# Performance work log

Hardware: AMD Instinct MI355X
Metric: run time of the kernel (lower is better)

The kernel has to match this reference:

```python
import jax, jax.numpy as jnp
import numpy as np
import math

D_MODEL = 512
N_HEADS = 8
D_FF = 2048
EPS = 1e-5

def _layernorm(x, g, b):
    m = jnp.mean(x, axis=-1, keepdims=True)
    v = jnp.var(x, axis=-1, keepdims=True)
    return (x - m) * jax.lax.rsqrt(v + EPS) * g + b

def setup_inputs() -> dict:
    key = jax.random.key(0)
    ks = jax.random.split(key, 8)
    d, dff = D_MODEL, D_FF
    s = lambda fan: 1.0 / math.sqrt(fan)
    return {
        "x": jax.random.normal(ks[0], (4, 2048, d), dtype=jnp.float32),
        "w_qkv": jax.random.normal(ks[1], (d, 3 * d), dtype=jnp.float32) * s(d),
        "b_qkv": jnp.zeros((3 * d,), dtype=jnp.float32),
        "w1": jax.random.normal(ks[2], (d, dff), dtype=jnp.float32) * s(d),
        "b1": jnp.zeros((dff,), dtype=jnp.float32),
        "w2": jax.random.normal(ks[3], (dff, d), dtype=jnp.float32) * s(dff),
        "b2": jnp.zeros((d,), dtype=jnp.float32),
        "g1": jnp.ones((d,), dtype=jnp.float32),
        "be1": jnp.zeros((d,), dtype=jnp.float32),
        "g2": jnp.ones((d,), dtype=jnp.float32),
        "be2": jnp.zeros((d,), dtype=jnp.float32),
    }

def reference(x, w_qkv, b_qkv, w1, b1, w2, b2, g1, be1, g2, be2):
    B, L, d = x.shape
    H = N_HEADS
    hd = d // H
    # Faithful to original: scale = 1/sqrt(hd), scores = qk / scale = qk * sqrt(hd)
    inv_scale = math.sqrt(hd)
    qkv = x @ w_qkv + b_qkv            # [B, L, 3d]
    q, k, v = jnp.split(qkv, 3, axis=-1)
    split_heads = lambda t: t.reshape(B, L, H, hd).transpose(0, 2, 1, 3)  # [B,H,L,hd]
    q, k, v = map(split_heads, (q, k, v))
    scores = jnp.einsum('bhqd,bhkd->bhqk', q, k) * inv_scale
    attn = jax.nn.softmax(scores, axis=-1)
    out = jnp.einsum('bhqk,bhkd->bhqd', attn, v)
    out = out.transpose(0, 2, 1, 3).reshape(B, L, d)
    x = _layernorm(x + out, g1, be1)
    ff = jax.nn.relu(x @ w1 + b1) @ w2 + b2
    return _layernorm(x + ff, g2, be2)
```

## Files before the change

kernel.cpp:

```cpp
#include <hip/hip_runtime.h>

typedef _Float16 f16;
typedef _Float16 f16x4 __attribute__((ext_vector_type(4)));
typedef _Float16 f16x8 __attribute__((ext_vector_type(8)));
typedef float    f32x4 __attribute__((ext_vector_type(4)));
typedef float    f32x16 __attribute__((ext_vector_type(16)));
typedef unsigned int u32x4 __attribute__((ext_vector_type(4)));

#define QK_SCALE 11.5416528f

__device__ __forceinline__ void g2l16(const void* g, void* l) {
  __builtin_amdgcn_global_load_lds(
      (__attribute__((address_space(1))) const unsigned int*)g,
      (__attribute__((address_space(3))) unsigned int*)l, 16, 0, 0);
}

__device__ __forceinline__ f32x4 mfma16(f16x8 a, f16x8 b, f32x4 c) {
  return __builtin_amdgcn_mfma_f32_16x16x32_f16(a, b, c, 0, 0, 0);
}
__device__ __forceinline__ f32x16 mfma32(f16x8 a, f16x8 b, f32x16 c) {
  return __builtin_amdgcn_mfma_f32_32x32x16_f16(a, b, c, 0, 0, 0);
}
__device__ __forceinline__ unsigned pkrtz(float a, float b) {
  auto t = __builtin_amdgcn_cvt_pkrtz(a, b);
  return *(unsigned*)&t;
}
__device__ __forceinline__ void swap32(unsigned& a, unsigned& b) {
  asm volatile("v_permlane32_swap_b32 %0, %1" : "+v"(a), "+v"(b));
}

#define WAIT_BARRIER(N)                                        \
  do {                                                         \
    asm volatile("s_waitcnt vmcnt(" #N ")" ::: "memory");      \
    __builtin_amdgcn_sched_barrier(0);                         \
    __builtin_amdgcn_s_barrier();                              \
    __builtin_amdgcn_sched_barrier(0);                         \
  } while (0)

__device__ __forceinline__ int swz64(int row, int c) { return row * 64 + ((c ^ (row & 7)) << 3); }
__device__ __forceinline__ int swz32(int row, int c) { return row * 32 + ((c ^ ((row >> 1) & 3)) << 3); }

__global__ __launch_bounds__(256) void k_split(const float* __restrict__ in,
                                               f16* __restrict__ hi, f16* __restrict__ lo, int n4) {
  int i = blockIdx.x * 256 + threadIdx.x;
  if (i >= n4) return;
  f32x4 v = ((const f32x4*)in)[i];
  f16x4 h, l;
#pragma unroll
  for (int j = 0; j < 4; ++j) {
    f16 hv = (f16)v[j];
    h[j] = hv;
    l[j] = (f16)(v[j] - (float)hv);
  }
  ((f16x4*)hi)[i] = h;
  ((f16x4*)lo)[i] = l;
}

template <bool WLO>
__global__ __launch_bounds__(256) void k_transpose_split(const float* __restrict__ in, int K, int N,
                                                         f16* __restrict__ oh, f16* __restrict__ ol) {
  __shared__ float t[32][33];
  const int tx = threadIdx.x, ty = threadIdx.y;
  const int n0 = blockIdx.x * 32, k0 = blockIdx.y * 32;
#pragma unroll
  for (int j = 0; j < 4; ++j)
    t[ty + j * 8][tx] = in[(size_t)(k0 + ty + j * 8) * N + n0 + tx];
  __syncthreads();
#pragma unroll
  for (int j = 0; j < 4; ++j) {
    float v = t[tx][ty + j * 8];
    f16 hv = (f16)v;
    size_t o = (size_t)(n0 + ty + j * 8) * K + k0 + tx;
    oh[o] = hv;
    if (WLO) ol[o] = (f16)(v - (float)hv);
  }
}

template <int EPI, bool SPLIT>
__global__ __launch_bounds__(256, SPLIT ? 2 : 3) void k_gemm(
    const f16* __restrict__ Ah, const f16* __restrict__ Al,
    const f16* __restrict__ Bh, const f16* __restrict__ Bl,
    const float* __restrict__ bias,
    f16* __restrict__ outH, f16* __restrict__ outH2,
    f16* __restrict__ oqh, f16* __restrict__ oql,
    f16* __restrict__ okh, f16* __restrict__ ovT,
    int M, int N, int K, int ks) {
  constexpr int NBUF = SPLIT ? 2 : 3;
  constexpr int NB = SPLIT ? 2 : 1;
  __shared__ f16 As[NBUF][NB][128 * 32];
  __shared__ f16 Bs[NBUF][NB][128 * 32];

  const int tid = threadIdx.x;
  const int bm = blockIdx.x, bn = blockIdx.y;
  const int bnc = (EPI == 3) ? (bn & 3) : bn;
  const int half = (EPI == 3) ? (bn >> 2) : 0;
  const int hoff = half * 1024;
  const int w = tid >> 6, lane = tid & 63;
  const int wr = w >> 1, wc = w & 1;
  const int lrow = lane & 15, lgrp = lane >> 4;

  const bool useLo = SPLIT && !(EPI == 0 && bn >= 4);

  f32x4 acc[4][4] = {};

  auto stg = [&](int bf, int kt) {
    const int kk = kt << 5;
#pragma unroll
    for (int c = 0; c < 2; ++c) {
      const int i = tid + (c << 8);
      const int row = i >> 2;
      const int gch = ((i & 3) ^ ((i >> 3) & 3)) << 3;
      const size_t aoff = (size_t)(bm * 128 + row) * ks + hoff + kk + gch;
      const size_t boff = (size_t)(bnc * 128 + row) * ks + hoff + kk + gch;
      g2l16(Ah + aoff, &As[bf][0][i * 8]);
      g2l16(Bh + boff, &Bs[bf][0][i * 8]);
      if (SPLIT)
        if (useLo) {
          g2l16(Al + aoff, &As[bf][1][i * 8]);
          g2l16(Bl + boff, &Bs[bf][1][i * 8]);
        }
    }
  };

  auto compute = [&](int bf) {
    f16x8 a0[4], a1[4], b0[4], b1[4];
#pragma unroll
    for (int mf = 0; mf < 4; ++mf) {
      const int off = swz32(wr * 64 + mf * 16 + lrow, lgrp);
      a0[mf] = *(const f16x8*)&As[bf][0][off];
      if (SPLIT)
        if (useLo) a1[mf] = *(const f16x8*)&As[bf][SPLIT ? 1 : 0][off];
    }
#pragma unroll
    for (int nf = 0; nf < 4; ++nf) {
      const int off = swz32(wc * 64 + nf * 16 + lrow, lgrp);
      b0[nf] = *(const f16x8*)&Bs[bf][0][off];
      if (SPLIT)
        if (useLo) b1[nf] = *(const f16x8*)&Bs[bf][SPLIT ? 1 : 0][off];
    }
#pragma unroll
    for (int mf = 0; mf < 4; ++mf)
#pragma unroll
      for (int nf = 0; nf < 4; ++nf) {
        acc[mf][nf] = mfma16(a0[mf], b0[nf], acc[mf][nf]);
        if (SPLIT)
          if (useLo) {
            acc[mf][nf] = mfma16(a0[mf], b1[nf], acc[mf][nf]);
            acc[mf][nf] = mfma16(a1[mf], b0[nf], acc[mf][nf]);
          }
      }
  };

  const int nkt = K >> 5;
  if constexpr (!SPLIT) {
    stg(0, 0);
    stg(1, 1);
    WAIT_BARRIER(4);
    for (int kt = 0; kt < nkt; ++kt) {
      const int cur = kt % 3;
      const bool more2 = (kt + 2 < nkt);
      if (more2) stg((kt + 2) % 3, kt + 2);
      compute(cur);
      if (kt + 1 < nkt) {
        if (more2) WAIT_BARRIER(4);
        else       WAIT_BARRIER(0);
      }
    }
  } else {
    stg(0, 0);
    WAIT_BARRIER(0);
    for (int kt = 0; kt < nkt; ++kt) {
      const int cur = kt & 1;
      if (kt + 1 < nkt) stg(cur ^ 1, kt + 1);
      compute(cur);
      if (kt + 1 < nkt) WAIT_BARRIER(0);
    }
  }

  const int rowbase = bm * 128 + wr * 64 + lgrp * 4;
  const int colbase = bnc * 128 + wc * 64 + lrow;
#pragma unroll
  for (int mf = 0; mf < 4; ++mf) {
#pragma unroll
    for (int nf = 0; nf < 4; ++nf) {
      const int gc = colbase + nf * 16;
      const float bv = (EPI == 3 && half) ? 0.f : bias[gc];
#pragma unroll
      for (int r = 0; r < 4; ++r) {
        const int gr = rowbase + mf * 16 + r;
        const float val = acc[mf][nf][r] + bv;
        if (EPI == 0) {
          const int bb = gr >> 11, tok = gr & 2047;
          const int kind = gc >> 9, hh = (gc >> 6) & 7, dd = gc & 63;
          const size_t bhp = (size_t)((bb << 3) + hh);
          const size_t qidx = (bhp * 2048 + tok) * 64 + dd;
          if (kind == 0) {
            const float sv = val * QK_SCALE;
            const f16 hv = (f16)sv;
            oqh[qidx] = hv; oql[qidx] = (f16)(sv - (float)hv);
          } else if (kind == 1) {
            okh[qidx] = (f16)val;
          } else {
            ovT[(bhp * 64 + dd) * 2048 + tok] = (f16)val;
          }
        } else if (EPI == 1) {
          outH[(size_t)gr * N + gc] = (f16)fmaxf(val, 0.f);
        } else {
          f16* o = half ? outH2 : outH;
          o[(size_t)gr * N + gc] = (f16)val;
        }
      }
    }
  }
}

__global__ __launch_bounds__(256, 2) void k_attn(
    const f16* __restrict__ Qh, const f16* __restrict__ Ql,
    const f16* __restrict__ Kh, const f16* __restrict__ Vt,
    f16* __restrict__ out) {
  __shared__ f16 sK[4][64 * 64], sV[4][64 * 64];

  const int tid = threadIdx.x;
  const int wg = (blockIdx.x & 7) * 64 + (blockIdx.x >> 3);
  const int bh = wg >> 4, qt = wg & 15;
  const int w = tid >> 6, lane = tid & 63;
  const int lh = lane & 31, hh = lane >> 5;

  const int qrow = qt * 128 + w * 32 + lh;
  const size_t qoff = ((size_t)bh * 2048 + qrow) * 64;
  f16x8 qh8[4], ql8[4];
#pragma unroll
  for (int d = 0; d < 4; ++d) {
    const size_t o = qoff + d * 16 + hh * 8;
    qh8[d] = *(const f16x8*)(Qh + o);
    ql8[d] = *(const f16x8*)(Ql + o);
  }

  auto stage = [&](int b, int kt) {
    const size_t koff = ((size_t)bh * 2048 + (size_t)kt * 64) * 64;
    const size_t voff = (size_t)bh * 64 * 2048 + (size_t)kt * 64;
#pragma unroll
    for (int c = 0; c < 2; ++c) {
      const int i = tid + (c << 8);
      const int row = i >> 3;
      const int gch = ((i & 7) ^ (row & 7)) << 3;
      g2l16(Kh + koff + (size_t)row * 64 + gch, &sK[b][i * 8]);
      g2l16(Vt + voff + (size_t)row * 2048 + gch, &sV[b][i * 8]);
    }
  };

  stage(0, 0);
  stage(1, 1);

  float m_run = -3e38f;
  float l_run = 0.f;
  f32x16 oacc[2] = {};
  const f32x16 kZero = {};
  f32x16 sA[2] = {}, sB[2] = {};

  auto qk = [&](f32x16 (&s)[2], int bi) {
    __builtin_amdgcn_s_setprio(1);
    {
      const f16x8 k0 = *(const f16x8*)&sK[bi][swz64(lh, hh)];
      const f16x8 k1 = *(const f16x8*)&sK[bi][swz64(32 + lh, hh)];
      s[0] = mfma32(k0, qh8[0], kZero);
      s[0] = mfma32(k0, ql8[0], s[0]);
      s[1] = mfma32(k1, qh8[0], kZero);
      s[1] = mfma32(k1, ql8[0], s[1]);
    }
#pragma unroll
    for (int d = 1; d < 4; ++d) {
      const f16x8 k0 = *(const f16x8*)&sK[bi][swz64(lh, d * 2 + hh)];
      const f16x8 k1 = *(const f16x8*)&sK[bi][swz64(32 + lh, d * 2 + hh)];
      s[0] = mfma32(k0, qh8[d], s[0]);
      s[0] = mfma32(k0, ql8[d], s[0]);
      s[1] = mfma32(k1, qh8[d], s[1]);
      s[1] = mfma32(k1, ql8[d], s[1]);
    }
    __builtin_amdgcn_s_setprio(0);
  };

  auto sm_pv = [&](f32x16 (&s)[2], int bi) {
    float mt = s[0][0];
#pragma unroll
    for (int r = 0; r < 16; ++r) { mt = fmaxf(mt, s[0][r]); mt = fmaxf(mt, s[1][r]); }
    mt = fmaxf(mt, __shfl_xor(mt, 32, 64));
    float mcur = m_run;
    if (!__all(mt <= mcur + 8.0f)) {
      const float mnew = fmaxf(mcur, mt);
      const float corr = __builtin_amdgcn_exp2f(mcur - mnew);
      m_run = mnew;
      l_run *= corr;
      oacc[0] = oacc[0] * corr;
      oacc[1] = oacc[1] * corr;
      mcur = mnew;
    }
    float ps = 0.f;
    unsigned pk0[8], pk1[8];
#pragma unroll
    for (int i = 0; i < 8; ++i) {
      const float a0 = __builtin_amdgcn_exp2f(s[0][2 * i] - mcur);
      const float a1 = __builtin_amdgcn_exp2f(s[0][2 * i + 1] - mcur);
      const float b0 = __builtin_amdgcn_exp2f(s[1][2 * i] - mcur);
      const float b1 = __builtin_amdgcn_exp2f(s[1][2 * i + 1] - mcur);
      ps += (a0 + a1) + (b0 + b1);
      pk0[i] = pkrtz(a0, a1);
      pk1[i] = pkrtz(b0, b1);
    }
    ps += __shfl_xor(ps, 32, 64);
    l_run += ps;

    swap32(pk0[0], pk0[2]); swap32(pk0[1], pk0[3]);
    swap32(pk0[4], pk0[6]); swap32(pk0[5], pk0[7]);
    swap32(pk1[0], pk1[2]); swap32(pk1[1], pk1[3]);
    swap32(pk1[4], pk1[6]); swap32(pk1[5], pk1[7]);

    u32x4 pbu[4];
    pbu[0] = (u32x4){pk0[0], pk0[1], pk0[2], pk0[3]};
    pbu[1] = (u32x4){pk0[4], pk0[5], pk0[6], pk0[7]};
    pbu[2] = (u32x4){pk1[0], pk1[1], pk1[2], pk1[3]};
    pbu[3] = (u32x4){pk1[4], pk1[5], pk1[6], pk1[7]};

    __builtin_amdgcn_s_setprio(1);
#pragma unroll
    for (int s2 = 0; s2 < 4; ++s2) {
      const f16x8 pb = *(const f16x8*)&pbu[s2];
#pragma unroll
      for (int db = 0; db < 2; ++db) {
        const f16x8 v = *(const f16x8*)&sV[bi][swz64(db * 32 + lh, s2 * 2 + hh)];
        oacc[db] = mfma32(v, pb, oacc[db]);
      }
    }
    __builtin_amdgcn_s_setprio(0);
  };

  WAIT_BARRIER(0);
  qk(sA, 0);

  for (int t = 0; t < 32; t += 2) {
    if (t + 2 < 32) {
      stage((t + 2) & 3, t + 2);
      stage((t + 3) & 3, t + 3);
    }
    qk(sB, (t + 1) & 3);
    sm_pv(sA, t & 3);
    sm_pv(sB, (t + 1) & 3);
    if (t + 2 < 32) {
      WAIT_BARRIER(0);
      qk(sA, (t + 2) & 3);
    }
  }

  const int b = bh >> 3, hd = bh & 7;
  const float inv = 1.0f / l_run;
  const int trow = b * 2048 + qt * 128 + w * 32 + lh;
  f16* po = out + (size_t)trow * 512 + hd * 64;
#pragma unroll
  for (int db = 0; db < 2; ++db)
#pragma unroll
    for (int rq = 0; rq < 4; ++rq) {
      f16x4 o;
#pragma unroll
      for (int j = 0; j < 4; ++j) o[j] = (f16)(oacc[db][rq * 4 + j] * inv);
      *(f16x4*)(po + db * 32 + rq * 8 + hh * 4) = o;
    }
}

__global__ __launch_bounds__(256) void k_ln1(const float* __restrict__ X, const f16* __restrict__ R,
                                             const float* __restrict__ g, const float* __restrict__ be,
                                             f16* __restrict__ outH) {
  const int row = blockIdx.x * 4 + (threadIdx.x >> 6);
  const int t = threadIdx.x & 63;
  const size_t base = (size_t)row * 512 + t * 8;
  f32x4 x0 = *(const f32x4*)(X + base);
  f32x4 x1 = *(const f32x4*)(X + base + 4);
  const f16x8 r = *(const f16x8*)(R + base);
#pragma unroll
  for (int j = 0; j < 4; ++j) { x0[j] += (float)r[j]; x1[j] += (float)r[j + 4]; }
  float s = 0.f, ss = 0.f;
#pragma unroll
  for (int j = 0; j < 4; ++j) { s += x0[j] + x1[j]; ss += x0[j] * x0[j] + x1[j] * x1[j]; }
#pragma unroll
  for (int o = 32; o; o >>= 1) {
    s += __shfl_xor(s, o, 64);
    ss += __shfl_xor(ss, o, 64);
  }
  const float mean = s * (1.f / 512.f);
  const float var = ss * (1.f / 512.f) - mean * mean;
  const float rs = rsqrtf(var + 1e-5f);
  f32x4 g0 = *(const f32x4*)(g + t * 8);
  f32x4 g1v = *(const f32x4*)(g + t * 8 + 4);
  f32x4 b0 = *(const f32x4*)(be + t * 8);
  f32x4 b1 = *(const f32x4*)(be + t * 8 + 4);
  f16x8 hx;
#pragma unroll
  for (int j = 0; j < 4; ++j) {
    hx[j] = (f16)((x0[j] - mean) * rs * g0[j] + b0[j]);
    hx[j + 4] = (f16)((x1[j] - mean) * rs * g1v[j] + b1[j]);
  }
  *(f16x8*)(outH + base) = hx;
}

__global__ __launch_bounds__(256) void k_ln2(const f16* __restrict__ Xh,
                                             const f16* __restrict__ R0, const f16* __restrict__ R1,
                                             const float* __restrict__ g, const float* __restrict__ be,
                                             float* __restrict__ out) {
  const int row = blockIdx.x * 4 + (threadIdx.x >> 6);
  const int t = threadIdx.x & 63;
  const size_t base = (size_t)row * 512 + t * 8;
  const f16x8 xv = *(const f16x8*)(Xh + base);
  const f16x8 r0 = *(const f16x8*)(R0 + base);
  const f16x8 r1 = *(const f16x8*)(R1 + base);
  f32x4 x0, x1;
#pragma unroll
  for (int j = 0; j < 4; ++j) {
    x0[j] = (float)xv[j] + (float)r0[j] + (float)r1[j];
    x1[j] = (float)xv[j + 4] + (float)r0[j + 4] + (float)r1[j + 4];
  }
  float s = 0.f, ss = 0.f;
#pragma unroll
  for (int j = 0; j < 4; ++j) { s += x0[j] + x1[j]; ss += x0[j] * x0[j] + x1[j] * x1[j]; }
#pragma unroll
  for (int o = 32; o; o >>= 1) {
    s += __shfl_xor(s, o, 64);
    ss += __shfl_xor(ss, o, 64);
  }
  const float mean = s * (1.f / 512.f);
  const float var = ss * (1.f / 512.f) - mean * mean;
  const float rs = rsqrtf(var + 1e-5f);
  f32x4 g0 = *(const f32x4*)(g + t * 8);
  f32x4 g1v = *(const f32x4*)(g + t * 8 + 4);
  f32x4 b0 = *(const f32x4*)(be + t * 8);
  f32x4 b1 = *(const f32x4*)(be + t * 8 + 4);
  f32x4 y0 = (x0 - mean) * rs * g0 + b0;
  f32x4 y1 = (x1 - mean) * rs * g1v + b1;
  *(f32x4*)(out + base) = y0;
  *(f32x4*)(out + base + 4) = y1;
}

extern "C" void kernel_launch(void* const* d_in, const int* in_sizes, int n_in,
                              void* d_out, int out_size, void* d_ws, size_t ws_size,
                              hipStream_t stream) {
  (void)in_sizes; (void)n_in; (void)out_size;
  const float* x = (const float*)d_in[0];
  const float* w_qkv = (const float*)d_in[1];
  const float* b_qkv = (const float*)d_in[2];
  const float* w1 = (const float*)d_in[3];
  const float* b1 = (const float*)d_in[4];
  const float* w2 = (const float*)d_in[5];
  const float* b2 = (const float*)d_in[6];
  const float* g1 = (const float*)d_in[7];
  const float* be1 = (const float*)d_in[8];
  const float* g2 = (const float*)d_in[9];
  const float* be2 = (const float*)d_in[10];
  float* out = (float*)d_out;

  char* p = (char*)d_ws;
  auto take = [&](size_t bytes) {
    char* r = p;
    p += (bytes + 255) & ~(size_t)255;
    return r;
  };
  f16* xh = (f16*)take(8192ull * 512 * 2);
  f16* xl = (f16*)take(8192ull * 512 * 2);
  f16* wqkvTh = (f16*)take(1536ull * 512 * 2);
  f16* wqkvTl = (f16*)take(1536ull * 512 * 2);
  f16* w1T = (f16*)take(2048ull * 512 * 2);
  f16* w2T = (f16*)take(512ull * 2048 * 2);
  f16* qh = (f16*)take(32ull * 2048 * 64 * 2);
  f16* ql = (f16*)take(32ull * 2048 * 64 * 2);
  f16* kh = (f16*)take(32ull * 2048 * 64 * 2);
  f16* vT = (f16*)take(32ull * 64 * 2048 * 2);
  f16* attnH = (f16*)take(8192ull * 512 * 2);
  f16* x1h = (f16*)take(8192ull * 512 * 2);
  f16* ffb0 = (f16*)take(8192ull * 512 * 2);
  f16* ffb1 = (f16*)take(8192ull * 512 * 2);
  f16* hbuf = qh;

  if ((size_t)(p - (char*)d_ws) > ws_size) return;

  dim3 tb(32, 8);
  k_split<<<4096, 256, 0, stream>>>(x, xh, xl, 8192 * 512 / 4);
  k_transpose_split<true><<<dim3(1536 / 32, 512 / 32), tb, 0, stream>>>(w_qkv, 512, 1536, wqkvTh, wqkvTl);
  k_transpose_split<false><<<dim3(2048 / 32, 512 / 32), tb, 0, stream>>>(w1, 512, 2048, w1T, nullptr);
  k_transpose_split<false><<<dim3(512 / 32, 2048 / 32), tb, 0, stream>>>(w2, 2048, 512, w2T, nullptr);

  k_gemm<0, true><<<dim3(64, 12), 256, 0, stream>>>(xh, xl, wqkvTh, wqkvTl, b_qkv,
                                                    nullptr, nullptr, qh, ql, kh, vT,
                                                    8192, 1536, 512, 512);
  k_attn<<<512, 256, 0, stream>>>(qh, ql, kh, vT, attnH);
  k_ln1<<<2048, 256, 0, stream>>>(x, attnH, g1, be1, x1h);
  k_gemm<1, false><<<dim3(64, 16), 256, 0, stream>>>(x1h, nullptr, w1T, nullptr, b1,
                                                     hbuf, nullptr, nullptr, nullptr, nullptr, nullptr,
                                                     8192, 2048, 512, 512);
  k_gemm<3, false><<<dim3(64, 8), 256, 0, stream>>>(hbuf, nullptr, w2T, nullptr, b2,
                                                    ffb0, ffb1, nullptr, nullptr, nullptr, nullptr,
                                                    8192, 512, 1024, 2048);
  k_ln2<<<2048, 256, 0, stream>>>(x1h, ffb0, ffb1, g2, be2, out);
}
```

Before: 198.7 us.

## Deepen attention K/V prefetch pipeline and simplify GEMM to double buffering

In the attention kernel, three K/V tiles are now prefetched up front and each half-iteration issues one new stage, with partial vmcnt waits so loads stay in flight across barriers instead of draining everything each pair of tiles. The non-split GEMM drops its triple-buffered pipeline and uses the same double-buffered loop with full __syncthreads as the split path. This cuts LDS use for that GEMM, which may allow more blocks per CU, but it gives up prefetch depth and adds a barrier every k-step. The finer attention waits need the vmcnt counts to match the per-stage load count, or results can race.

```diff
diff --git a/kernel.cpp b/kernel.cpp
--- a/kernel.cpp
+++ b/kernel.cpp
@@ -85,10 +85,9 @@
     f16* __restrict__ oqh, f16* __restrict__ oql,
     f16* __restrict__ okh, f16* __restrict__ ovT,
     int M, int N, int K, int ks) {
-  constexpr int NBUF = SPLIT ? 2 : 3;
   constexpr int NB = SPLIT ? 2 : 1;
-  __shared__ f16 As[NBUF][NB][128 * 32];
-  __shared__ f16 Bs[NBUF][NB][128 * 32];
+  __shared__ f16 As[2][NB][128 * 32];
+  __shared__ f16 Bs[2][NB][128 * 32];
 
   const int tid = threadIdx.x;
   const int bm = blockIdx.x, bn = blockIdx.y;
@@ -152,29 +151,13 @@
   };
 
   const int nkt = K >> 5;
-  if constexpr (!SPLIT) {
-    stg(0, 0);
-    stg(1, 1);
-    WAIT_BARRIER(4);
-    for (int kt = 0; kt < nkt; ++kt) {
-      const int cur = kt % 3;
-      const bool more2 = (kt + 2 < nkt);
-      if (more2) stg((kt + 2) % 3, kt + 2);
-      compute(cur);
-      if (kt + 1 < nkt) {
-        if (more2) WAIT_BARRIER(4);
-        else       WAIT_BARRIER(0);
-      }
-    }
-  } else {
-    stg(0, 0);
-    WAIT_BARRIER(0);
-    for (int kt = 0; kt < nkt; ++kt) {
-      const int cur = kt & 1;
-      if (kt + 1 < nkt) stg(cur ^ 1, kt + 1);
-      compute(cur);
-      if (kt + 1 < nkt) WAIT_BARRIER(0);
-    }
+  stg(0, 0);
+  __syncthreads();
+  for (int kt = 0; kt < nkt; ++kt) {
+    const int cur = kt & 1;
+    if (kt + 1 < nkt) stg(cur ^ 1, kt + 1);
+    compute(cur);
+    __syncthreads();
   }
 
   const int rowbase = bm * 128 + wr * 64 + lgrp * 4;
@@ -251,6 +234,7 @@
 
   stage(0, 0);
   stage(1, 1);
+  stage(2, 2);
 
   float m_run = -3e38f;
   float l_run = 0.f;
@@ -334,20 +318,35 @@
     __builtin_amdgcn_s_setprio(0);
   };
 
-  WAIT_BARRIER(0);
+  auto endwait = [&](int t) {
+    if (t < 29) {
+      asm volatile("s_waitcnt vmcnt(4)" ::: "memory");
+    } else {
+      asm volatile("s_waitcnt vmcnt(0)" ::: "memory");
+    }
+    __builtin_amdgcn_sched_barrier(0);
+    __builtin_amdgcn_s_barrier();
+    __builtin_amdgcn_sched_barrier(0);
+  };
+
+  asm volatile("s_waitcnt vmcnt(4)" ::: "memory");
+  __builtin_amdgcn_sched_barrier(0);
+  __builtin_amdgcn_s_barrier();
+  __builtin_amdgcn_sched_barrier(0);
   qk(sA, 0);
 
   for (int t = 0; t < 32; t += 2) {
-    if (t + 2 < 32) {
-      stage((t + 2) & 3, t + 2);
-      stage((t + 3) & 3, t + 3);
-    }
-    qk(sB, (t + 1) & 3);
-    sm_pv(sA, t & 3);
-    sm_pv(sB, (t + 1) & 3);
-    if (t + 2 < 32) {
-      WAIT_BARRIER(0);
-      qk(sA, (t + 2) & 3);
+    {
+      if (t + 1 < 32) qk(sB, (t + 1) & 3);
+      if (t + 3 < 32) stage((t + 3) & 3, t + 3);
+      sm_pv(sA, t & 3);
+      if (t + 1 < 32) endwait(t);
+    }
+    if (t + 1 < 32) {
+      if (t + 2 < 32) qk(sA, (t + 2) & 3);
+      if (t + 4 < 32) stage((t + 4) & 3, t + 4);
+      sm_pv(sB, (t + 1) & 3);
+      if (t + 2 < 32) endwait(t + 1);
     }
   }
 
```

Result: faster. 190.4 us (-4.2%).
